# Kernel tuning notes

Measured on AMD Instinct MI355X. Metric: run time of the kernel, lower is better.

Reference implementation:

```python
import jax, jax.numpy as jnp
import numpy as np

NEG_POS_RATIO = 3
B, P, C = 128, 8732, 21  # batch, SSD300 priors, VOC classes (hardcoded 21 in original)


def setup_inputs() -> dict:
    key = jax.random.key(0)
    k1, k2, k3, k4, k5, k6 = jax.random.split(key, 6)
    confidence = jax.random.normal(k1, (B, P, C), jnp.float32)
    predicted_locations = jax.random.normal(k2, (B, P, 4), jnp.float32)
    gt_locations = jax.random.normal(k3, (B, P, 4), jnp.float32)
    raw_labels = jax.random.randint(k4, (B, P), 0, C)
    keep = jax.random.uniform(k5, (B, P)) < 0.03
    labels = jnp.where(keep, raw_labels, 0).astype(jnp.int64)
    mask = jax.random.uniform(k6, (B, P), jnp.float32)
    return {
        "confidence": confidence,
        "predicted_locations": predicted_locations,
        "labels": labels,
        "gt_locations": gt_locations,
        "mask": mask,
    }


def _hard_negative_mining(bg_loss, labels, neg_pos_ratio):
    # Faithful to SSD box_utils.hard_negative_mining.
    pos_mask = labels > 0                                   # [B,P] bool
    num_pos = pos_mask.sum(axis=1, keepdims=True)           # [B,1]
    num_neg = num_pos * neg_pos_ratio                       # [B,1]
    masked = jnp.where(pos_mask, -jnp.inf, bg_loss)         # positives excluded
    idx = jnp.argsort(-masked, axis=1)                      # descending by loss
    orders = jnp.argsort(idx, axis=1)                       # rank of each prior
    neg_mask = orders < num_neg                             # top num_neg hardest
    return pos_mask, neg_mask


def reference(confidence, predicted_locations, labels, gt_locations, mask):
    nls = -jax.nn.log_softmax(confidence, axis=-1)          # [B,P,C]
    bg_loss = nls[:, :, 0]                                  # [B,P]
    pos_mask, neg_mask = _hard_negative_mining(bg_loss, labels, NEG_POS_RATIO)
    posf = pos_mask.astype(nls.dtype)

    # per-prior NLL at the assigned label, weighted by mask over positives
    per_label = jnp.take_along_axis(nls, labels[..., None], axis=2)[..., 0]  # [B,P]
    confidence_pos_loss = (mask * per_label * posf).sum()
    confidence_neg_loss = jnp.where(neg_mask, bg_loss, 0.0).sum()
    confidence_loss = confidence_pos_loss + confidence_neg_loss

    # smooth-L1 over positive priors, weighted by mask (broadcast over 4 coords)
    d = predicted_locations - gt_locations                  # [B,P,4]
    ad = jnp.abs(d)
    sl1 = jnp.where(ad < 1.0, 0.5 * d * d, ad - 0.5)
    regression_loss = (sl1 * (mask * posf)[..., None]).sum()

    all_batch_pos = mask.sum()
    return regression_loss / all_batch_pos, confidence_loss / all_batch_pos
```

## Files before the change

### kernel.cpp

```cpp
#include <hip/hip_runtime.h>
#include <stdint.h>

#define BATCH 128
#define PRI   8732
#define NCLS  21
#define NPR   3
#define TOTAL (BATCH * PRI)
#define CPB   4
#define NBLK  (TOTAL / (256 * CPB))


__global__ __launch_bounds__(256, 6)
void k_main(const float* __restrict__ conf, const float* __restrict__ pred,
            const int* __restrict__ labels, const float* __restrict__ gt,
            const float* __restrict__ mask, uint32_t* __restrict__ keys,
            float* __restrict__ pm, float* __restrict__ pp, float* __restrict__ pr)
{
  __shared__ float sconf[256 * NCLS];
  __shared__ float sm_[4], sp_[4], sr_[4];
  const int tid = threadIdx.x;
  const long long blk_base = (long long)blockIdx.x * (256 * CPB);

  float4 pf[6];
  {
    const float4* src = (const float4*)(conf + blk_base * NCLS);
    #pragma unroll
    for (int i = 0; i < 5; ++i) pf[i] = src[i * 256 + tid];
    if (tid < 64) pf[5] = src[1280 + tid];
  }
  int   lab = labels[blk_base + tid];
  float mk  = mask  [blk_base + tid];

  float accm = 0.f, accp = 0.f, accr = 0.f;

  #pragma unroll 1
  for (int ch = 0; ch < CPB; ++ch) {
    const long long cbase = blk_base + (long long)ch * 256;

    float4* dst = (float4*)sconf;
    #pragma unroll
    for (int i = 0; i < 5; ++i) dst[i * 256 + tid] = pf[i];
    if (tid < 64) dst[1280 + tid] = pf[5];
    __syncthreads();

    const long long a = cbase + tid;
    const int   clab = lab;
    const float cmk  = mk;

    if (ch + 1 < CPB) {
      const float4* nsrc = (const float4*)(conf + (cbase + 256) * NCLS);
      #pragma unroll
      for (int i = 0; i < 5; ++i) pf[i] = nsrc[i * 256 + tid];
      if (tid < 64) pf[5] = nsrc[1280 + tid];
      lab = labels[a + 256];
      mk  = mask  [a + 256];
    }

    const float* cv = &sconf[tid * NCLS];
    float m = cv[0];
    #pragma unroll
    for (int c = 1; c < NCLS; ++c) m = fmaxf(m, cv[c]);
    float s = 0.f;
    #pragma unroll
    for (int c = 0; c < NCLS; ++c) s += __expf(cv[c] - m);
    const float lse = m + __logf(s);
    const float bg  = lse - cv[0];
    const bool  pos = clab > 0;

    accm += cmk;
    if (pos) {
      accp += cmk * (lse - cv[clab]);
      const float4 pd = ((const float4*)pred)[a];
      const float4 g  = ((const float4*)gt)[a];
      float sl = 0.f, d, ad;
      d = pd.x - g.x; ad = fabsf(d); sl += (ad < 1.f) ? 0.5f * d * d : ad - 0.5f;
      d = pd.y - g.y; ad = fabsf(d); sl += (ad < 1.f) ? 0.5f * d * d : ad - 0.5f;
      d = pd.z - g.z; ad = fabsf(d); sl += (ad < 1.f) ? 0.5f * d * d : ad - 0.5f;
      d = pd.w - g.w; ad = fabsf(d); sl += (ad < 1.f) ? 0.5f * d * d : ad - 0.5f;
      accr += cmk * sl;
    }
    keys[a] = pos ? 0u : (__float_as_uint(bg) | 0x80000000u);
    __syncthreads();
  }

  #pragma unroll
  for (int o = 32; o > 0; o >>= 1) {
    accm += __shfl_down(accm, o);
    accp += __shfl_down(accp, o);
    accr += __shfl_down(accr, o);
  }
  const int w = tid >> 6;
  if ((tid & 63) == 0) { sm_[w] = accm; sp_[w] = accp; sr_[w] = accr; }
  __syncthreads();
  if (tid == 0) {
    pm[blockIdx.x] = sm_[0] + sm_[1] + sm_[2] + sm_[3];
    pp[blockIdx.x] = sp_[0] + sp_[1] + sp_[2] + sp_[3];
    pr[blockIdx.x] = sr_[0] + sr_[1] + sr_[2] + sr_[3];
  }
}

#define SEL_T 512
#define RPT   18

__global__ __launch_bounds__(SEL_T)
void k_select(const uint32_t* __restrict__ keys, double* __restrict__ neg)
{
  __shared__ int    slots[16 * 24 + 8];
  __shared__ int    ired[8];
  __shared__ double dred[8];
  const int tid  = threadIdx.x;
  const int w    = tid >> 6;
  const int lane = tid & 63;
  const uint32_t* row = keys + (size_t)blockIdx.x * PRI;

  uint32_t kr[RPT];
  #pragma unroll
  for (int r = 0; r < 17; ++r) kr[r] = row[tid + 512 * r];
  kr[17] = (tid < 28) ? row[tid + 8704] : 0u;

  int zc = 0;
  #pragma unroll
  for (int r = 0; r < 17; ++r) zc += (kr[r] == 0u) ? 1 : 0;
  if (tid < 28) zc += (kr[17] == 0u) ? 1 : 0;
  #pragma unroll
  for (int o = 32; o > 0; o >>= 1) zc += __shfl_down(zc, o);
  if (lane == 0) ired[w] = zc;
  __syncthreads();
  int np = 0;
  #pragma unroll
  for (int i = 0; i < 8; ++i) np += ired[i];

  int k = np * NPR;
  const int nneg = PRI - np;
  if (k > nneg) k = nneg;

  double result = 0.0;
  if (k > 0) {
    uint32_t cur = 0x80000000u;
    #pragma unroll 1
    for (int bit = 30; bit >= 1; bit -= 2) {
      const int rnd = (30 - bit) >> 1;
      const uint32_t tA = cur | (3u << (bit - 1));
      const uint32_t tB = cur | (1u << bit);
      const uint32_t tC = cur | (1u << (bit - 1));
      int cA = 0, cB = 0, cC = 0;
      #pragma unroll
      for (int r = 0; r < RPT; ++r) {
        cA += (int)__popcll(__ballot(kr[r] >= tA));
        cB += (int)__popcll(__ballot(kr[r] >= tB));
        cC += (int)__popcll(__ballot(kr[r] >= tC));
      }
      if (lane == 0) {
        int* sl = &slots[rnd * 24];
        sl[w] = cA; sl[8 + w] = cB; sl[16 + w] = cC;
      }
      __syncthreads();
      int TA = 0, TB = 0, TC = 0;
      const int* sl = &slots[rnd * 24];
      #pragma unroll
      for (int i = 0; i < 8; ++i) { TA += sl[i]; TB += sl[8 + i]; TC += sl[16 + i]; }
      cur = (TA >= k) ? tA : (TB >= k) ? tB : (TC >= k) ? tC : cur;
    }
    {
      const uint32_t t = cur | 1u;
      int c = 0;
      #pragma unroll
      for (int r = 0; r < RPT; ++r) c += (int)__popcll(__ballot(kr[r] >= t));
      if (lane == 0) slots[16 * 24 + w] = c;
      __syncthreads();
      int tot = 0;
      #pragma unroll
      for (int i = 0; i < 8; ++i) tot += slots[16 * 24 + i];
      if (tot >= k) cur = t;
    }

    const float thr = __uint_as_float(cur & 0x7fffffffu);
    double ssum = 0.0;
    int g = 0;
    #pragma unroll
    for (int r = 0; r < RPT; ++r) {
      if (kr[r] > cur) { ssum += (double)__uint_as_float(kr[r] & 0x7fffffffu); ++g; }
    }
    #pragma unroll
    for (int o = 32; o > 0; o >>= 1) { ssum += __shfl_down(ssum, o); g += __shfl_down(g, o); }
    if (lane == 0) { dred[w] = ssum; ired[w] = g; }
    __syncthreads();
    if (tid == 0) {
      double tot = 0.0; int gg = 0;
      #pragma unroll
      for (int i = 0; i < 8; ++i) { tot += dred[i]; gg += ired[i]; }
      result = tot + (double)(k - gg) * (double)thr;
    }
  }
  if (tid == 0) neg[blockIdx.x] = result;
}

__global__ __launch_bounds__(256)
void k_final(const float* __restrict__ pm, const float* __restrict__ pp,
             const float* __restrict__ pr, const double* __restrict__ neg,
             float* __restrict__ out)
{
  __shared__ double red[4][4];
  const int tid = threadIdx.x, w = tid >> 6, lane = tid & 63;
  double sm = 0.0, sp = 0.0, sr = 0.0, sn = 0.0;
  for (int i = tid; i < NBLK; i += 256) {
    sm += (double)pm[i]; sp += (double)pp[i]; sr += (double)pr[i];
  }
  if (tid < BATCH) sn = neg[tid];
  #pragma unroll
  for (int o = 32; o > 0; o >>= 1) {
    sm += __shfl_down(sm, o); sp += __shfl_down(sp, o);
    sr += __shfl_down(sr, o); sn += __shfl_down(sn, o);
  }
  if (lane == 0) { red[0][w] = sm; red[1][w] = sp; red[2][w] = sr; red[3][w] = sn; }
  __syncthreads();
  if (tid == 0) {
    double m = 0, p = 0, r = 0, n = 0;
    #pragma unroll
    for (int i = 0; i < 4; ++i) { m += red[0][i]; p += red[1][i]; r += red[2][i]; n += red[3][i]; }
    out[0] = (float)(r / m);
    out[1] = (float)((p + n) / m);
  }
}

extern "C" void kernel_launch(void* const* d_in, const int* in_sizes, int n_in,
                              void* d_out, int out_size, void* d_ws, size_t ws_size,
                              hipStream_t stream) {
  const float* conf   = (const float*)d_in[0];
  const float* pred   = (const float*)d_in[1];
  const int*   labels = (const int*)d_in[2];
  const float* gt     = (const float*)d_in[3];
  const float* mask   = (const float*)d_in[4];
  float* out = (float*)d_out;

  char* ws = (char*)d_ws;
  const size_t keys_bytes = (size_t)TOTAL * sizeof(uint32_t);
  uint32_t* keys = (uint32_t*)ws;
  float*  pm  = (float*)(ws + keys_bytes);
  float*  pp  = pm + NBLK;
  float*  pr  = pp + NBLK;
  double* neg = (double*)(ws + keys_bytes + ((3 * NBLK * sizeof(float) + 7) & ~(size_t)7));

  k_main<<<NBLK, 256, 0, stream>>>(conf, pred, labels, gt, mask, keys, pm, pp, pr);
  k_select<<<BATCH, SEL_T, 0, stream>>>(keys, neg);
  k_final<<<1, 256, 0, stream>>>(pm, pp, pr, neg, out);
}
```

Baseline: 214.1 us.

## Load confidence tiles directly into LDS and use one chunk per block

Replaces the register-staged, software-prefetched 4-chunk loop with direct global-to-LDS loads via global_load_lds, and launches one 256-prior chunk per block, so there are four times as many blocks. This removes the register round trip and the extra LDS store pass, and relies on higher occupancy rather than explicit prefetch to hide latency. In exchange it produces more per-block partial sums for the final reduction and loses the in-block overlap between loading the next chunk and computing the current one.

```diff
diff --git a/kernel.cpp b/kernel.cpp
--- a/kernel.cpp
+++ b/kernel.cpp
@@ -6,82 +6,70 @@
 #define NCLS  21
 #define NPR   3
 #define TOTAL (BATCH * PRI)
-#define CPB   4
-#define NBLK  (TOTAL / (256 * CPB))
-
-
-__global__ __launch_bounds__(256, 6)
+#define NBLK  (TOTAL / 256)
+
+
+typedef const __attribute__((address_space(1))) void gv_t;
+typedef __attribute__((address_space(3))) void lv_t;
+
+__global__ __launch_bounds__(256)
 void k_main(const float* __restrict__ conf, const float* __restrict__ pred,
             const int* __restrict__ labels, const float* __restrict__ gt,
             const float* __restrict__ mask, uint32_t* __restrict__ keys,
             float* __restrict__ pm, float* __restrict__ pp, float* __restrict__ pr)
 {
-  __shared__ float sconf[256 * NCLS];
+  __shared__ __align__(16) float sconf[256 * NCLS];
   __shared__ float sm_[4], sp_[4], sr_[4];
   const int tid = threadIdx.x;
-  const long long blk_base = (long long)blockIdx.x * (256 * CPB);
-
-  float4 pf[6];
-  {
-    const float4* src = (const float4*)(conf + blk_base * NCLS);
-    #pragma unroll
-    for (int i = 0; i < 5; ++i) pf[i] = src[i * 256 + tid];
-    if (tid < 64) pf[5] = src[1280 + tid];
-  }
-  int   lab = labels[blk_base + tid];
-  float mk  = mask  [blk_base + tid];
-
-  float accm = 0.f, accp = 0.f, accr = 0.f;
-
-  #pragma unroll 1
-  for (int ch = 0; ch < CPB; ++ch) {
-    const long long cbase = blk_base + (long long)ch * 256;
-
-    float4* dst = (float4*)sconf;
-    #pragma unroll
-    for (int i = 0; i < 5; ++i) dst[i * 256 + tid] = pf[i];
-    if (tid < 64) dst[1280 + tid] = pf[5];
-    __syncthreads();
-
-    const long long a = cbase + tid;
-    const int   clab = lab;
-    const float cmk  = mk;
-
-    if (ch + 1 < CPB) {
-      const float4* nsrc = (const float4*)(conf + (cbase + 256) * NCLS);
-      #pragma unroll
-      for (int i = 0; i < 5; ++i) pf[i] = nsrc[i * 256 + tid];
-      if (tid < 64) pf[5] = nsrc[1280 + tid];
-      lab = labels[a + 256];
-      mk  = mask  [a + 256];
-    }
-
-    const float* cv = &sconf[tid * NCLS];
-    float m = cv[0];
-    #pragma unroll
-    for (int c = 1; c < NCLS; ++c) m = fmaxf(m, cv[c]);
-    float s = 0.f;
-    #pragma unroll
-    for (int c = 0; c < NCLS; ++c) s += __expf(cv[c] - m);
-    const float lse = m + __logf(s);
-    const float bg  = lse - cv[0];
-    const bool  pos = clab > 0;
-
-    accm += cmk;
-    if (pos) {
-      accp += cmk * (lse - cv[clab]);
-      const float4 pd = ((const float4*)pred)[a];
-      const float4 g  = ((const float4*)gt)[a];
-      float sl = 0.f, d, ad;
-      d = pd.x - g.x; ad = fabsf(d); sl += (ad < 1.f) ? 0.5f * d * d : ad - 0.5f;
-      d = pd.y - g.y; ad = fabsf(d); sl += (ad < 1.f) ? 0.5f * d * d : ad - 0.5f;
-      d = pd.z - g.z; ad = fabsf(d); sl += (ad < 1.f) ? 0.5f * d * d : ad - 0.5f;
-      d = pd.w - g.w; ad = fabsf(d); sl += (ad < 1.f) ? 0.5f * d * d : ad - 0.5f;
-      accr += cmk * sl;
-    }
-    keys[a] = pos ? 0u : (__float_as_uint(bg) | 0x80000000u);
-    __syncthreads();
-  }
+  const int wv  = tid >> 6;
+  const int ln  = tid & 63;
+  const long long base = (long long)blockIdx.x * 256;
+  const float4* src4 = (const float4*)(conf + base * NCLS);
+
+  #pragma unroll
+  for (int i = 0; i < 5; ++i) {
+    __builtin_amdgcn_global_load_lds(
+        (gv_t*)(src4 + i * 256 + tid),
+        (lv_t*)((float4*)sconf + i * 256 + wv * 64),
+        16, 0, 0);
+  }
+  if (wv == 0) {
+    __builtin_amdgcn_global_load_lds(
+        (gv_t*)(src4 + 1280 + ln),
+        (lv_t*)((float4*)sconf + 1280),
+        16, 0, 0);
+  }
+
+  const long long a = base + tid;
+  const int   lab = labels[a];
+  const float mk  = mask[a];
+
+  __syncthreads();
+
+  const float* cv = &sconf[tid * NCLS];
+  float m = cv[0];
+  #pragma unroll
+  for (int c = 1; c < NCLS; ++c) m = fmaxf(m, cv[c]);
+  float s = 0.f;
+  #pragma unroll
+  for (int c = 0; c < NCLS; ++c) s += __expf(cv[c] - m);
+  const float lse = m + __logf(s);
+  const float bg  = lse - cv[0];
+  const bool  pos = lab > 0;
+
+  float accm = mk, accp = 0.f, accr = 0.f;
+  if (pos) {
+    accp = mk * (lse - cv[lab]);
+    const float4 pd = ((const float4*)pred)[a];
+    const float4 g  = ((const float4*)gt)[a];
+    float sl = 0.f, d, ad;
+    d = pd.x - g.x; ad = fabsf(d); sl += (ad < 1.f) ? 0.5f * d * d : ad - 0.5f;
+    d = pd.y - g.y; ad = fabsf(d); sl += (ad < 1.f) ? 0.5f * d * d : ad - 0.5f;
+    d = pd.z - g.z; ad = fabsf(d); sl += (ad < 1.f) ? 0.5f * d * d : ad - 0.5f;
+    d = pd.w - g.w; ad = fabsf(d); sl += (ad < 1.f) ? 0.5f * d * d : ad - 0.5f;
+    accr = mk * sl;
+  }
+  keys[a] = pos ? 0u : (__float_as_uint(bg) | 0x80000000u);
 
   #pragma unroll
   for (int o = 32; o > 0; o >>= 1) {
@@ -89,8 +77,7 @@
     accp += __shfl_down(accp, o);
     accr += __shfl_down(accr, o);
   }
-  const int w = tid >> 6;
-  if ((tid & 63) == 0) { sm_[w] = accm; sp_[w] = accp; sr_[w] = accr; }
+  if (ln == 0) { sm_[wv] = accm; sp_[wv] = accp; sr_[wv] = accr; }
   __syncthreads();
   if (tid == 0) {
     pm[blockIdx.x] = sm_[0] + sm_[1] + sm_[2] + sm_[3];
```

Result: faster. 193.6 us (-9.6%).
